# Kernel optimization log

Hardware: AMD Instinct MI355X
Metric: run time of the kernel (lower is better)

## Reference

```python
import jax, jax.numpy as jnp
import numpy as np
from jax import lax

B, S, D, H = 256, 512, 64, 128


def _cell(x, h, c, Wih, Whh, bih, bhh):
    # PyTorch LSTM gate layout: i, f, g, o
    g = x @ Wih.T + h @ Whh.T + (bih + bhh)
    i, f, gg, o = jnp.split(g, 4, axis=-1)
    c = jax.nn.sigmoid(f) * c + jax.nn.sigmoid(i) * jnp.tanh(gg)
    h = jax.nn.sigmoid(o) * jnp.tanh(c)
    return h, c


def _lstm_layer(xs, Wih, Whh, bih, bhh):
    # xs: [B, S, in] -> ys: [B, S, H], final (h, c): [B, H]
    b = xs.shape[0]
    h0 = jnp.zeros((b, H), xs.dtype)
    c0 = jnp.zeros((b, H), xs.dtype)

    def step(carry, xt):
        h, c = carry
        h, c = _cell(xt, h, c, Wih, Whh, bih, bhh)
        return (h, c), h

    (h, c), ys = lax.scan(step, (h0, c0), jnp.swapaxes(xs, 0, 1))
    return jnp.swapaxes(ys, 0, 1), h, c


def setup_inputs() -> dict:
    key = jax.random.key(0)
    ks = jax.random.split(key, 20)
    s = 1.0 / np.sqrt(H)
    p = {}
    p["x"] = jax.random.normal(ks[0], (B, S, D), jnp.float32)
    # encoder / decoder stacked LSTM params (layer 0 input=D, layer 1 input=H)
    idx = 1
    for pre in ["enc", "dec"]:
        for l, in_sz in [(0, D), (1, H)]:
            p[f"{pre}_Wih{l}"] = jax.random.uniform(ks[idx], (4 * H, in_sz), jnp.float32, -s, s); idx += 1
            p[f"{pre}_Whh{l}"] = jax.random.uniform(ks[idx], (4 * H, H), jnp.float32, -s, s); idx += 1
            p[f"{pre}_bih{l}"] = jax.random.uniform(ks[idx], (4 * H,), jnp.float32, -s, s); idx += 1
            p[f"{pre}_bhh{l}"] = jax.random.uniform(ks[idx], (4 * H,), jnp.float32, -s, s); idx += 1
    p["fc_W"] = jax.random.uniform(ks[17], (D, H), jnp.float32, -s, s)
    p["fc_b"] = jax.random.uniform(ks[18], (D,), jnp.float32, -s, s)
    return p


def reference(x, enc_Wih0, enc_Whh0, enc_bih0, enc_bhh0,
              enc_Wih1, enc_Whh1, enc_bih1, enc_bhh1,
              dec_Wih0, dec_Whh0, dec_bih0, dec_bhh0,
              dec_Wih1, dec_Whh1, dec_bih1, dec_bhh1,
              fc_W, fc_b):
    b, seq, d = x.shape
    # ---- Encoder: 2-layer LSTM (eval mode; inter-layer dropout disabled) ----
    y0, h0, c0 = _lstm_layer(x, enc_Wih0, enc_Whh0, enc_bih0, enc_bhh0)
    _, h1, c1 = _lstm_layer(y0, enc_Wih1, enc_Whh1, enc_bih1, enc_bhh1)

    def dec_step(carry, _):
        y, dh0, dc0, dh1, dc1 = carry
        dh0, dc0 = _cell(y, dh0, dc0, dec_Wih0, dec_Whh0, dec_bih0, dec_bhh0)
        dh1, dc1 = _cell(dh0, dh1, dc1, dec_Wih1, dec_Whh1, dec_bih1, dec_bhh1)
        pred = dh1 @ fc_W.T + fc_b
        return (pred, dh0, dc0, dh1, dc1), pred

    y_init = jnp.zeros((b, d), x.dtype)
    _, preds = lax.scan(dec_step, (y_init, h0, c0, h1, c1), None, length=seq)
    return jnp.swapaxes(preds, 0, 1)  # [B, S, D]
```

## Files before the change

### kernel.cpp

```cpp
#include <hip/hip_runtime.h>
#include <hip/hip_fp16.h>


typedef _Float16 h2 __attribute__((ext_vector_type(2)));
typedef _Float16 h8 __attribute__((ext_vector_type(8)));

#define Bsz 256
#define Ssz 512
#define Dsz 64
#define Hsz 128
#define G4 512
#define NT 512

__device__ __forceinline__ float fdot2f(h2 a, h2 b, float c) {
#if __has_builtin(__builtin_amdgcn_fdot2)
  return __builtin_amdgcn_fdot2(a, b, c, false);
#else
  return c + (float)a[0] * (float)b[0] + (float)a[1] * (float)b[1];
#endif
}

__device__ __forceinline__ float dot8(h8 v, h8 w, float acc) {
  h2 v0 = __builtin_shufflevector(v, v, 0, 1);
  h2 v1 = __builtin_shufflevector(v, v, 2, 3);
  h2 v2 = __builtin_shufflevector(v, v, 4, 5);
  h2 v3 = __builtin_shufflevector(v, v, 6, 7);
  h2 w0 = __builtin_shufflevector(w, w, 0, 1);
  h2 w1 = __builtin_shufflevector(w, w, 2, 3);
  h2 w2 = __builtin_shufflevector(w, w, 4, 5);
  h2 w3 = __builtin_shufflevector(w, w, 6, 7);
  acc = fdot2f(v0, w0, acc);
  acc = fdot2f(v1, w1, acc);
  acc = fdot2f(v2, w2, acc);
  acc = fdot2f(v3, w3, acc);
  return acc;
}

__device__ __forceinline__ float sigm(float v) { return 1.f / (1.f + __expf(-v)); }
__device__ __forceinline__ float tanh_f(float v) { return 2.f / (1.f + __expf(-2.f * v)) - 1.f; }

__global__ void __launch_bounds__(NT, 2)
enc_kernel(const float* __restrict__ x,
           const h8* __restrict__ wih0, const h8* __restrict__ whh0,
           const h8* __restrict__ wih1, const h8* __restrict__ whh1,
           const float* __restrict__ bsum0, const float* __restrict__ bsum1,
           float* __restrict__ st) {
  __shared__ h8 s_whh1[16 * G4];
  __shared__ float g[G4];
  __shared__ h8 hp0[16], hp1[16];
  __shared__ h8 xp[2][8];

  const int tid = threadIdx.x;
  const int row = blockIdx.x;

  h8 Wih0[8], Whh0[16], Wih1[16];
#pragma unroll
  for (int k = 0; k < 8; ++k) Wih0[k] = wih0[k * G4 + tid];
#pragma unroll
  for (int k = 0; k < 16; ++k) Whh0[k] = whh0[k * G4 + tid];
#pragma unroll
  for (int k = 0; k < 16; ++k) Wih1[k] = wih1[k * G4 + tid];
  for (int i = tid; i < 16 * G4; i += NT) s_whh1[i] = whh1[i];

  if (tid < 128) ((_Float16*)hp0)[tid] = (_Float16)0.f;
  else if (tid < 256) ((_Float16*)hp1)[tid - 128] = (_Float16)0.f;
  else if (tid < 320) {
    int j = tid - 256;
    ((_Float16*)xp[0])[j] = (_Float16)x[(size_t)row * Ssz * Dsz + j];
  }
  const float b0 = bsum0[tid];
  const float b1 = bsum1[tid];
  float c_reg = 0.f, h_last = 0.f;
  __syncthreads();

  for (int t = 0; t < Ssz; ++t) {
    {
      float a[4] = {b0, 0.f, 0.f, 0.f};
#pragma unroll
      for (int k = 0; k < 8; ++k) a[k & 3] = dot8(xp[t & 1][k], Wih0[k], a[k & 3]);
#pragma unroll
      for (int k = 0; k < 16; ++k) a[k & 3] = dot8(hp0[k], Whh0[k], a[k & 3]);
      g[4 * (tid & 127) + (tid >> 7)] = (a[0] + a[1]) + (a[2] + a[3]);
    }
    __syncthreads();
    if (tid < 128) {
      const float4 gv = *(const float4*)&g[4 * tid];
      float ig = sigm(gv.x), fg = sigm(gv.y), gg = tanh_f(gv.z), og = sigm(gv.w);
      c_reg = fg * c_reg + ig * gg;
      float h = og * tanh_f(c_reg);
      h_last = h;
      ((_Float16*)hp0)[tid] = (_Float16)h;
    } else if (tid >= 256 && tid < 320) {
      if (t + 1 < Ssz) {
        int j = tid - 256;
        ((_Float16*)xp[(t + 1) & 1])[j] =
            (_Float16)x[((size_t)row * Ssz + (t + 1)) * Dsz + j];
      }
    }
    __syncthreads();
    {
      float a[4] = {b1, 0.f, 0.f, 0.f};
#pragma unroll
      for (int k = 0; k < 16; ++k) a[k & 3] = dot8(hp0[k], Wih1[k], a[k & 3]);
#pragma unroll
      for (int k = 0; k < 16; ++k) a[k & 3] = dot8(hp1[k], s_whh1[k * G4 + tid], a[k & 3]);
      g[4 * (tid & 127) + (tid >> 7)] = (a[0] + a[1]) + (a[2] + a[3]);
    }
    __syncthreads();
    if (tid >= 128 && tid < 256) {
      int j = tid - 128;
      const float4 gv = *(const float4*)&g[4 * j];
      float ig = sigm(gv.x), fg = sigm(gv.y), gg = tanh_f(gv.z), og = sigm(gv.w);
      c_reg = fg * c_reg + ig * gg;
      float h = og * tanh_f(c_reg);
      h_last = h;
      ((_Float16*)hp1)[j] = (_Float16)h;
    }
    __syncthreads();
  }

  if (tid < 128) {
    st[0 * Bsz * Hsz + row * Hsz + tid] = h_last;
    st[1 * Bsz * Hsz + row * Hsz + tid] = c_reg;
  } else if (tid < 256) {
    int j = tid - 128;
    st[2 * Bsz * Hsz + row * Hsz + j] = h_last;
    st[3 * Bsz * Hsz + row * Hsz + j] = c_reg;
  }
}

__global__ void __launch_bounds__(NT, 2)
dec_kernel(const h8* __restrict__ wih0, const h8* __restrict__ whh0,
           const h8* __restrict__ wih1, const h8* __restrict__ whh1,
           const h8* __restrict__ fcp,
           const float* __restrict__ bsum0, const float* __restrict__ bsum1,
           const float* __restrict__ fcb, const float* __restrict__ st,
           float* __restrict__ out) {
  __shared__ h8 s_whh1[16 * G4];
  __shared__ h8 s_fc[16 * Dsz];
  __shared__ float g[G4];
  __shared__ h8 hp0[16], hp1[16], yp[8];

  const int tid = threadIdx.x;
  const int row = blockIdx.x;

  h8 Wih0[8], Whh0[16], Wih1[16];
#pragma unroll
  for (int k = 0; k < 8; ++k) Wih0[k] = wih0[k * G4 + tid];
#pragma unroll
  for (int k = 0; k < 16; ++k) Whh0[k] = whh0[k * G4 + tid];
#pragma unroll
  for (int k = 0; k < 16; ++k) Wih1[k] = wih1[k * G4 + tid];
  for (int i = tid; i < 16 * G4; i += NT) s_whh1[i] = whh1[i];
  for (int i = tid; i < 16 * Dsz; i += NT) s_fc[i] = fcp[i];

  float c_reg = 0.f;
  if (tid < 128) {
    float h0v = st[0 * Bsz * Hsz + row * Hsz + tid];
    c_reg = st[1 * Bsz * Hsz + row * Hsz + tid];
    ((_Float16*)hp0)[tid] = (_Float16)h0v;
  } else if (tid < 256) {
    int j = tid - 128;
    float h1v = st[2 * Bsz * Hsz + row * Hsz + j];
    c_reg = st[3 * Bsz * Hsz + row * Hsz + j];
    ((_Float16*)hp1)[j] = (_Float16)h1v;
  } else if (tid < 320) {
    ((_Float16*)yp)[tid - 256] = (_Float16)0.f;
  }
  const float b0 = bsum0[tid];
  const float b1 = bsum1[tid];
  const float fb = (tid < Dsz) ? fcb[tid] : 0.f;
  __syncthreads();

  for (int t = 0; t < Ssz; ++t) {
    {
      float a[4] = {b0, 0.f, 0.f, 0.f};
#pragma unroll
      for (int k = 0; k < 8; ++k) a[k & 3] = dot8(yp[k], Wih0[k], a[k & 3]);
#pragma unroll
      for (int k = 0; k < 16; ++k) a[k & 3] = dot8(hp0[k], Whh0[k], a[k & 3]);
      g[4 * (tid & 127) + (tid >> 7)] = (a[0] + a[1]) + (a[2] + a[3]);
    }
    __syncthreads();
    if (tid < 128) {
      const float4 gv = *(const float4*)&g[4 * tid];
      float ig = sigm(gv.x), fg = sigm(gv.y), gg = tanh_f(gv.z), og = sigm(gv.w);
      c_reg = fg * c_reg + ig * gg;
      float h = og * tanh_f(c_reg);
      ((_Float16*)hp0)[tid] = (_Float16)h;
    }
    __syncthreads();
    {
      float a[4] = {b1, 0.f, 0.f, 0.f};
#pragma unroll
      for (int k = 0; k < 16; ++k) a[k & 3] = dot8(hp0[k], Wih1[k], a[k & 3]);
#pragma unroll
      for (int k = 0; k < 16; ++k) a[k & 3] = dot8(hp1[k], s_whh1[k * G4 + tid], a[k & 3]);
      g[4 * (tid & 127) + (tid >> 7)] = (a[0] + a[1]) + (a[2] + a[3]);
    }
    __syncthreads();
    if (tid >= 128 && tid < 256) {
      int j = tid - 128;
      const float4 gv = *(const float4*)&g[4 * j];
      float ig = sigm(gv.x), fg = sigm(gv.y), gg = tanh_f(gv.z), og = sigm(gv.w);
      c_reg = fg * c_reg + ig * gg;
      float h = og * tanh_f(c_reg);
      ((_Float16*)hp1)[j] = (_Float16)h;
    }
    __syncthreads();
    if (tid < Dsz) {
      float a[2] = {fb, 0.f};
#pragma unroll
      for (int k = 0; k < 16; ++k) a[k & 1] = dot8(hp1[k], s_fc[k * Dsz + tid], a[k & 1]);
      float v = a[0] + a[1];
      out[((size_t)row * Ssz + t) * Dsz + tid] = v;
      ((_Float16*)yp)[tid] = (_Float16)v;
    }
    __syncthreads();
  }
}

__global__ void pack8_kernel(const float* __restrict__ W, h8* __restrict__ o, int K, int N) {
  int idx = blockIdx.x * 256 + threadIdx.x;
  int tot = (K >> 3) * N;
  if (idx >= tot) return;
  int k8 = idx / N, n = idx - k8 * N;
  const float* p = W + n * K + 8 * k8;
  h8 v;
#pragma unroll
  for (int j = 0; j < 8; ++j) v[j] = (_Float16)p[j];
  o[idx] = v;
}

__global__ void addb_kernel(const float* __restrict__ a, const float* __restrict__ b,
                            float* __restrict__ o, int n) {
  int i = blockIdx.x * 256 + threadIdx.x;
  if (i < n) o[i] = a[i] + b[i];
}

extern "C" void kernel_launch(void* const* d_in, const int* in_sizes, int n_in,
                              void* d_out, int out_size, void* d_ws, size_t ws_size,
                              hipStream_t stream) {
  (void)in_sizes; (void)n_in; (void)out_size; (void)ws_size;
  char* ws = (char*)d_ws;
  size_t off = 0;
  auto take = [&](size_t bytes) {
    char* p = ws + off;
    off += (bytes + 255) & ~(size_t)255;
    return p;
  };

  h8* e0_wih = (h8*)take(8 * 512 * 16);
  h8* e0_whh = (h8*)take(16 * 512 * 16);
  h8* e1_wih = (h8*)take(16 * 512 * 16);
  h8* e1_whh = (h8*)take(16 * 512 * 16);
  h8* d0_wih = (h8*)take(8 * 512 * 16);
  h8* d0_whh = (h8*)take(16 * 512 * 16);
  h8* d1_wih = (h8*)take(16 * 512 * 16);
  h8* d1_whh = (h8*)take(16 * 512 * 16);
  h8* fcp    = (h8*)take(16 * 64 * 16);
  float* bs_e0 = (float*)take(512 * 4);
  float* bs_e1 = (float*)take(512 * 4);
  float* bs_d0 = (float*)take(512 * 4);
  float* bs_d1 = (float*)take(512 * 4);
  float* st    = (float*)take(4 * Bsz * Hsz * 4);

  const float* x = (const float*)d_in[0];

  struct PW { const float* w; h8* o; int K, N; };
  PW pw[9] = {
    {(const float*)d_in[1],  e0_wih, 64, 512},
    {(const float*)d_in[2],  e0_whh, 128, 512},
    {(const float*)d_in[5],  e1_wih, 128, 512},
    {(const float*)d_in[6],  e1_whh, 128, 512},
    {(const float*)d_in[9],  d0_wih, 64, 512},
    {(const float*)d_in[10], d0_whh, 128, 512},
    {(const float*)d_in[13], d1_wih, 128, 512},
    {(const float*)d_in[14], d1_whh, 128, 512},
    {(const float*)d_in[17], fcp, 128, 64},
  };
  for (int i = 0; i < 9; ++i) {
    int tot = (pw[i].K >> 3) * pw[i].N;
    pack8_kernel<<<(tot + 255) / 256, 256, 0, stream>>>(pw[i].w, pw[i].o, pw[i].K, pw[i].N);
  }
  addb_kernel<<<2, 256, 0, stream>>>((const float*)d_in[3],  (const float*)d_in[4],  bs_e0, 512);
  addb_kernel<<<2, 256, 0, stream>>>((const float*)d_in[7],  (const float*)d_in[8],  bs_e1, 512);
  addb_kernel<<<2, 256, 0, stream>>>((const float*)d_in[11], (const float*)d_in[12], bs_d0, 512);
  addb_kernel<<<2, 256, 0, stream>>>((const float*)d_in[15], (const float*)d_in[16], bs_d1, 512);

  enc_kernel<<<Bsz, NT, 0, stream>>>(x, e0_wih, e0_whh, e1_wih, e1_whh, bs_e0, bs_e1, st);
  dec_kernel<<<Bsz, NT, 0, stream>>>(d0_wih, d0_whh, d1_wih, d1_whh, fcp, bs_d0, bs_d1,
                                     (const float*)d_in[18], st, (float*)d_out);
}
```

Baseline: 2.339 ms.

## Fold FC into decoder input weights and compute gates with DPP lane exchange

New measurement: 6.362 ms. 2.72x slower.

```diff
diff --git a/kernel.cpp b/kernel.cpp
--- a/kernel.cpp
+++ b/kernel.cpp
@@ -39,203 +39,251 @@
 __device__ __forceinline__ float sigm(float v) { return 1.f / (1.f + __expf(-v)); }
 __device__ __forceinline__ float tanh_f(float v) { return 2.f / (1.f + __expf(-2.f * v)) - 1.f; }
 
+template <int C, int M>
+__device__ __forceinline__ float qperm(float x) {
+#if __has_builtin(__builtin_amdgcn_mov_dpp)
+  int i = __builtin_amdgcn_mov_dpp(__builtin_bit_cast(int, x), C, 0xf, 0xf, true);
+  return __builtin_bit_cast(float, i);
+#else
+  return __shfl_xor(x, M, 64);
+#endif
+}
+
+__device__ __forceinline__ int permcol(int n) { return (n & 3) * 128 + (n >> 2); }
+
 __global__ void __launch_bounds__(NT, 2)
 enc_kernel(const float* __restrict__ x,
            const h8* __restrict__ wih0, const h8* __restrict__ whh0,
            const h8* __restrict__ wih1, const h8* __restrict__ whh1,
-           const float* __restrict__ bsum0, const float* __restrict__ bsum1,
+           const float* __restrict__ b0v, const float* __restrict__ b1v,
            float* __restrict__ st) {
-  __shared__ h8 s_whh1[16 * G4];
-  __shared__ float g[G4];
-  __shared__ h8 hp0[16], hp1[16];
-  __shared__ h8 xp[2][8];
+  __shared__ h8 s_wih0[8 * G4];
+  __shared__ h8 H0[2][16], H1[2][16], xp[2][8];
 
   const int tid = threadIdx.x;
   const int row = blockIdx.x;
-
-  h8 Wih0[8], Whh0[16], Wih1[16];
-#pragma unroll
-  for (int k = 0; k < 8; ++k) Wih0[k] = wih0[k * G4 + tid];
+  const int r = tid & 3;
+  const int j = tid >> 2;
+
+  h8 Whh0[16], Wih1[16], Whh1[16];
 #pragma unroll
   for (int k = 0; k < 16; ++k) Whh0[k] = whh0[k * G4 + tid];
 #pragma unroll
   for (int k = 0; k < 16; ++k) Wih1[k] = wih1[k * G4 + tid];
-  for (int i = tid; i < 16 * G4; i += NT) s_whh1[i] = whh1[i];
-
-  if (tid < 128) ((_Float16*)hp0)[tid] = (_Float16)0.f;
-  else if (tid < 256) ((_Float16*)hp1)[tid - 128] = (_Float16)0.f;
-  else if (tid < 320) {
-    int j = tid - 256;
-    ((_Float16*)xp[0])[j] = (_Float16)x[(size_t)row * Ssz * Dsz + j];
-  }
-  const float b0 = bsum0[tid];
-  const float b1 = bsum1[tid];
-  float c_reg = 0.f, h_last = 0.f;
+#pragma unroll
+  for (int k = 0; k < 16; ++k) Whh1[k] = whh1[k * G4 + tid];
+  for (int i = tid; i < 8 * G4; i += NT) s_wih0[i] = wih0[i];
+
+  if (tid < 128) ((_Float16*)H0[0])[tid] = (_Float16)0.f;
+  else if (tid < 256) ((_Float16*)H1[0])[tid - 128] = (_Float16)0.f;
+  else if (tid < 320)
+    ((_Float16*)xp[0])[tid - 256] = (_Float16)x[(size_t)row * Ssz * Dsz + (tid - 256)];
+
+  const float b0 = b0v[tid], b1 = b1v[tid];
+  const float Sc = (r == 2) ? 2.f : 1.f;
+  const float Kc = (r == 2) ? 2.f : 1.f;
+  const float Dc = (r == 2) ? -1.f : 0.f;
+  float c0 = 0.f, c1 = 0.f, h0_last = 0.f, h1_last = 0.f;
   __syncthreads();
 
   for (int t = 0; t < Ssz; ++t) {
-    {
-      float a[4] = {b0, 0.f, 0.f, 0.f};
-#pragma unroll
-      for (int k = 0; k < 8; ++k) a[k & 3] = dot8(xp[t & 1][k], Wih0[k], a[k & 3]);
-#pragma unroll
-      for (int k = 0; k < 16; ++k) a[k & 3] = dot8(hp0[k], Whh0[k], a[k & 3]);
-      g[4 * (tid & 127) + (tid >> 7)] = (a[0] + a[1]) + (a[2] + a[3]);
+    const h8* H0r = H0[t & 1];
+    h8* H0w = H0[(t + 1) & 1];
+    float xv = 0.f;
+    const bool pf = (tid < Dsz) && (t + 1 < Ssz);
+    if (pf) xv = x[((size_t)row * Ssz + (t + 1)) * Dsz + tid];
+    float a = b0;
+#pragma unroll
+    for (int k = 0; k < 8; ++k) a = dot8(xp[t & 1][k], s_wih0[k * G4 + tid], a);
+#pragma unroll
+    for (int k = 0; k < 16; ++k) a = dot8(H0r[k], Whh0[k], a);
+    if (pf) ((_Float16*)xp[(t + 1) & 1])[tid] = (_Float16)xv;
+    float n = Sc * sigm(Kc * a) + Dc;
+    float vf = qperm<0xB1, 1>(n), vg = qperm<0x4E, 2>(n), vo = qperm<0x1B, 3>(n);
+    if (r == 0) {
+      c0 = vf * c0 + n * vg;
+      float h = vo * tanh_f(c0);
+      h0_last = h;
+      ((_Float16*)H0w)[j] = (_Float16)h;
     }
     __syncthreads();
-    if (tid < 128) {
-      const float4 gv = *(const float4*)&g[4 * tid];
-      float ig = sigm(gv.x), fg = sigm(gv.y), gg = tanh_f(gv.z), og = sigm(gv.w);
-      c_reg = fg * c_reg + ig * gg;
-      float h = og * tanh_f(c_reg);
-      h_last = h;
-      ((_Float16*)hp0)[tid] = (_Float16)h;
-    } else if (tid >= 256 && tid < 320) {
-      if (t + 1 < Ssz) {
-        int j = tid - 256;
-        ((_Float16*)xp[(t + 1) & 1])[j] =
-            (_Float16)x[((size_t)row * Ssz + (t + 1)) * Dsz + j];
-      }
-    }
-    __syncthreads();
-    {
-      float a[4] = {b1, 0.f, 0.f, 0.f};
-#pragma unroll
-      for (int k = 0; k < 16; ++k) a[k & 3] = dot8(hp0[k], Wih1[k], a[k & 3]);
-#pragma unroll
-      for (int k = 0; k < 16; ++k) a[k & 3] = dot8(hp1[k], s_whh1[k * G4 + tid], a[k & 3]);
-      g[4 * (tid & 127) + (tid >> 7)] = (a[0] + a[1]) + (a[2] + a[3]);
-    }
-    __syncthreads();
-    if (tid >= 128 && tid < 256) {
-      int j = tid - 128;
-      const float4 gv = *(const float4*)&g[4 * j];
-      float ig = sigm(gv.x), fg = sigm(gv.y), gg = tanh_f(gv.z), og = sigm(gv.w);
-      c_reg = fg * c_reg + ig * gg;
-      float h = og * tanh_f(c_reg);
-      h_last = h;
-      ((_Float16*)hp1)[j] = (_Float16)h;
-    }
-    __syncthreads();
-  }
-
-  if (tid < 128) {
-    st[0 * Bsz * Hsz + row * Hsz + tid] = h_last;
-    st[1 * Bsz * Hsz + row * Hsz + tid] = c_reg;
-  } else if (tid < 256) {
-    int j = tid - 128;
-    st[2 * Bsz * Hsz + row * Hsz + j] = h_last;
-    st[3 * Bsz * Hsz + row * Hsz + j] = c_reg;
+    const h8* H1r = H1[t & 1];
+    h8* H1w = H1[(t + 1) & 1];
+    float a1 = b1;
+#pragma unroll
+    for (int k = 0; k < 16; ++k) a1 = dot8(H0w[k], Wih1[k], a1);
+#pragma unroll
+    for (int k = 0; k < 16; ++k) a1 = dot8(H1r[k], Whh1[k], a1);
+    n = Sc * sigm(Kc * a1) + Dc;
+    vf = qperm<0xB1, 1>(n); vg = qperm<0x4E, 2>(n); vo = qperm<0x1B, 3>(n);
+    if (r == 0) {
+      c1 = vf * c1 + n * vg;
+      float h = vo * tanh_f(c1);
+      h1_last = h;
+      ((_Float16*)H1w)[j] = (_Float16)h;
+    }
+  }
+  if (r == 0) {
+    st[0 * Bsz * Hsz + row * Hsz + j] = h0_last;
+    st[1 * Bsz * Hsz + row * Hsz + j] = c0;
+    st[2 * Bsz * Hsz + row * Hsz + j] = h1_last;
+    st[3 * Bsz * Hsz + row * Hsz + j] = c1;
   }
 }
 
 __global__ void __launch_bounds__(NT, 2)
-dec_kernel(const h8* __restrict__ wih0, const h8* __restrict__ whh0,
+dec_kernel(const h8* __restrict__ wprime, const h8* __restrict__ whh0,
            const h8* __restrict__ wih1, const h8* __restrict__ whh1,
-           const h8* __restrict__ fcp,
-           const float* __restrict__ bsum0, const float* __restrict__ bsum1,
-           const float* __restrict__ fcb, const float* __restrict__ st,
-           float* __restrict__ out) {
+           const h8* __restrict__ fcpk,
+           const float* __restrict__ b00v, const float* __restrict__ b0tv,
+           const float* __restrict__ b1v, const float* __restrict__ fcb,
+           const float* __restrict__ st, float* __restrict__ out) {
   __shared__ h8 s_whh1[16 * G4];
-  __shared__ h8 s_fc[16 * Dsz];
-  __shared__ float g[G4];
-  __shared__ h8 hp0[16], hp1[16], yp[8];
+  __shared__ h8 H0[2][16], H1[2][16];
 
   const int tid = threadIdx.x;
   const int row = blockIdx.x;
-
-  h8 Wih0[8], Whh0[16], Wih1[16];
-#pragma unroll
-  for (int k = 0; k < 8; ++k) Wih0[k] = wih0[k * G4 + tid];
+  const int r = tid & 3;
+  const int j = tid >> 2;
+  const int j8 = tid >> 3;
+  const int kp = (tid & 7) * 2;
+
+  h8 Wp[16], Whh0[16], Wih1[16];
+#pragma unroll
+  for (int k = 0; k < 16; ++k) Wp[k] = wprime[k * G4 + tid];
 #pragma unroll
   for (int k = 0; k < 16; ++k) Whh0[k] = whh0[k * G4 + tid];
 #pragma unroll
   for (int k = 0; k < 16; ++k) Wih1[k] = wih1[k * G4 + tid];
+  const h8 Fc0 = fcpk[tid * 2];
+  const h8 Fc1 = fcpk[tid * 2 + 1];
   for (int i = tid; i < 16 * G4; i += NT) s_whh1[i] = whh1[i];
-  for (int i = tid; i < 16 * Dsz; i += NT) s_fc[i] = fcp[i];
-
-  float c_reg = 0.f;
-  if (tid < 128) {
-    float h0v = st[0 * Bsz * Hsz + row * Hsz + tid];
-    c_reg = st[1 * Bsz * Hsz + row * Hsz + tid];
-    ((_Float16*)hp0)[tid] = (_Float16)h0v;
-  } else if (tid < 256) {
-    int j = tid - 128;
-    float h1v = st[2 * Bsz * Hsz + row * Hsz + j];
-    c_reg = st[3 * Bsz * Hsz + row * Hsz + j];
-    ((_Float16*)hp1)[j] = (_Float16)h1v;
-  } else if (tid < 320) {
-    ((_Float16*)yp)[tid - 256] = (_Float16)0.f;
-  }
-  const float b0 = bsum0[tid];
-  const float b1 = bsum1[tid];
-  const float fb = (tid < Dsz) ? fcb[tid] : 0.f;
+
+  float c0 = 0.f, c1 = 0.f;
+  if (tid < 128)
+    ((_Float16*)H0[0])[tid] = (_Float16)st[0 * Bsz * Hsz + row * Hsz + tid];
+  else if (tid < 256)
+    ((_Float16*)H1[0])[tid - 128] = (_Float16)st[2 * Bsz * Hsz + row * Hsz + (tid - 128)];
+  if (r == 0) {
+    c0 = st[1 * Bsz * Hsz + row * Hsz + j];
+    c1 = st[3 * Bsz * Hsz + row * Hsz + j];
+  }
+  const float b00 = b00v[tid], b0t = b0tv[tid], b1 = b1v[tid];
+  const float fcbj = fcb[j8];
+  const float Sc = (r == 2) ? 2.f : 1.f;
+  const float Kc = (r == 2) ? 2.f : 1.f;
+  const float Dc = (r == 2) ? -1.f : 0.f;
   __syncthreads();
 
   for (int t = 0; t < Ssz; ++t) {
-    {
-      float a[4] = {b0, 0.f, 0.f, 0.f};
-#pragma unroll
-      for (int k = 0; k < 8; ++k) a[k & 3] = dot8(yp[k], Wih0[k], a[k & 3]);
-#pragma unroll
-      for (int k = 0; k < 16; ++k) a[k & 3] = dot8(hp0[k], Whh0[k], a[k & 3]);
-      g[4 * (tid & 127) + (tid >> 7)] = (a[0] + a[1]) + (a[2] + a[3]);
+    const h8* H0r = H0[t & 1];
+    h8* H0w = H0[(t + 1) & 1];
+    const h8* H1r = H1[t & 1];
+    float a;
+    if (t > 0) {
+      a = b0t;
+#pragma unroll
+      for (int k = 0; k < 16; ++k) a = dot8(H1r[k], Wp[k], a);
+      float op = dot8(H1r[kp], Fc0, 0.f);
+      op = dot8(H1r[kp + 1], Fc1, op);
+      op += __shfl_xor(op, 1);
+      op += __shfl_xor(op, 2);
+      op += __shfl_xor(op, 4);
+      if ((tid & 7) == 0)
+        out[((size_t)row * Ssz + (t - 1)) * Dsz + j8] = op + fcbj;
+    } else {
+      a = b00;
+    }
+#pragma unroll
+    for (int k = 0; k < 16; ++k) a = dot8(H0r[k], Whh0[k], a);
+    float n = Sc * sigm(Kc * a) + Dc;
+    float vf = qperm<0xB1, 1>(n), vg = qperm<0x4E, 2>(n), vo = qperm<0x1B, 3>(n);
+    if (r == 0) {
+      c0 = vf * c0 + n * vg;
+      ((_Float16*)H0w)[j] = (_Float16)(vo * tanh_f(c0));
     }
     __syncthreads();
-    if (tid < 128) {
-      const float4 gv = *(const float4*)&g[4 * tid];
-      float ig = sigm(gv.x), fg = sigm(gv.y), gg = tanh_f(gv.z), og = sigm(gv.w);
-      c_reg = fg * c_reg + ig * gg;
-      float h = og * tanh_f(c_reg);
-      ((_Float16*)hp0)[tid] = (_Float16)h;
+    h8* H1w = H1[(t + 1) & 1];
+    float a1 = b1;
+#pragma unroll
+    for (int k = 0; k < 16; ++k) a1 = dot8(H0w[k], Wih1[k], a1);
+#pragma unroll
+    for (int k = 0; k < 16; ++k) a1 = dot8(H1r[k], s_whh1[k * G4 + tid], a1);
+    n = Sc * sigm(Kc * a1) + Dc;
+    vf = qperm<0xB1, 1>(n); vg = qperm<0x4E, 2>(n); vo = qperm<0x1B, 3>(n);
+    if (r == 0) {
+      c1 = vf * c1 + n * vg;
+      ((_Float16*)H1w)[j] = (_Float16)(vo * tanh_f(c1));
     }
     __syncthreads();
-    {
-      float a[4] = {b1, 0.f, 0.f, 0.f};
-#pragma unroll
-      for (int k = 0; k < 16; ++k) a[k & 3] = dot8(hp0[k], Wih1[k], a[k & 3]);
-#pragma unroll
-      for (int k = 0; k < 16; ++k) a[k & 3] = dot8(hp1[k], s_whh1[k * G4 + tid], a[k & 3]);
-      g[4 * (tid & 127) + (tid >> 7)] = (a[0] + a[1]) + (a[2] + a[3]);
-    }
-    __syncthreads();
-    if (tid >= 128 && tid < 256) {
-      int j = tid - 128;
-      const float4 gv = *(const float4*)&g[4 * j];
-      float ig = sigm(gv.x), fg = sigm(gv.y), gg = tanh_f(gv.z), og = sigm(gv.w);
-      c_reg = fg * c_reg + ig * gg;
-      float h = og * tanh_f(c_reg);
-      ((_Float16*)hp1)[j] = (_Float16)h;
-    }
-    __syncthreads();
-    if (tid < Dsz) {
-      float a[2] = {fb, 0.f};
-#pragma unroll
-      for (int k = 0; k < 16; ++k) a[k & 1] = dot8(hp1[k], s_fc[k * Dsz + tid], a[k & 1]);
-      float v = a[0] + a[1];
-      out[((size_t)row * Ssz + t) * Dsz + tid] = v;
-      ((_Float16*)yp)[tid] = (_Float16)v;
-    }
-    __syncthreads();
-  }
-}
-
-__global__ void pack8_kernel(const float* __restrict__ W, h8* __restrict__ o, int K, int N) {
+  }
+  const h8* H1f = H1[Ssz & 1];
+  float op = dot8(H1f[kp], Fc0, 0.f);
+  op = dot8(H1f[kp + 1], Fc1, op);
+  op += __shfl_xor(op, 1);
+  op += __shfl_xor(op, 2);
+  op += __shfl_xor(op, 4);
+  if ((tid & 7) == 0)
+    out[((size_t)row * Ssz + (Ssz - 1)) * Dsz + j8] = op + fcbj;
+}
+
+
+__global__ void pack8p_kernel(const float* __restrict__ W, h8* __restrict__ o, int K) {
   int idx = blockIdx.x * 256 + threadIdx.x;
-  int tot = (K >> 3) * N;
+  int tot = (K >> 3) * G4;
   if (idx >= tot) return;
-  int k8 = idx / N, n = idx - k8 * N;
-  const float* p = W + n * K + 8 * k8;
+  int k8 = idx >> 9, np = idx & 511;
+  const float* p = W + permcol(np) * K + 8 * k8;
   h8 v;
 #pragma unroll
-  for (int j = 0; j < 8; ++j) v[j] = (_Float16)p[j];
+  for (int e = 0; e < 8; ++e) v[e] = (_Float16)p[e];
   o[idx] = v;
 }
 
-__global__ void addb_kernel(const float* __restrict__ a, const float* __restrict__ b,
-                            float* __restrict__ o, int n) {
-  int i = blockIdx.x * 256 + threadIdx.x;
-  if (i < n) o[i] = a[i] + b[i];
+__global__ void wprime_kernel(const float* __restrict__ wih0d, const float* __restrict__ fcw,
+                              h8* __restrict__ o) {
+  int idx = blockIdx.x * 256 + threadIdx.x;
+  if (idx >= 16 * G4) return;
+  int k8 = idx >> 9, np = idx & 511;
+  int col = permcol(np);
+  h8 v;
+#pragma unroll
+  for (int e = 0; e < 8; ++e) {
+    int h = 8 * k8 + e;
+    float s = 0.f;
+    for (int d = 0; d < 64; ++d) s += wih0d[col * 64 + d] * fcw[d * 128 + h];
+    v[e] = (_Float16)s;
+  }
+  o[idx] = v;
+}
+
+__global__ void fcpack_kernel(const float* __restrict__ fcw, h8* __restrict__ o) {
+  int idx = blockIdx.x * 256 + threadIdx.x;
+  if (idx >= 2 * NT) return;
+  int tt = idx >> 1, c = idx & 1;
+  int jj = tt >> 3, k = (tt & 7) * 2 + c;
+  h8 v;
+#pragma unroll
+  for (int e = 0; e < 8; ++e) v[e] = (_Float16)fcw[jj * 128 + k * 8 + e];
+  o[idx] = v;
+}
+
+__global__ void biasp_kernel(const float* __restrict__ a, const float* __restrict__ b,
+                             float* __restrict__ o) {
+  int n = blockIdx.x * 256 + threadIdx.x;
+  if (n >= G4) return;
+  int c = permcol(n);
+  o[n] = a[c] + b[c];
+}
+
+__global__ void bprime_kernel(const float* __restrict__ b00, const float* __restrict__ wih0d,
+                              const float* __restrict__ fcb, float* __restrict__ o) {
+  int n = blockIdx.x * 256 + threadIdx.x;
+  if (n >= G4) return;
+  int c = permcol(n);
+  float s = 0.f;
+  for (int d = 0; d < 64; ++d) s += fcb[d] * wih0d[c * 64 + d];
+  o[n] = b00[n] + s;
 }
 
 extern "C" void kernel_launch(void* const* d_in, const int* in_sizes, int n_in,
@@ -254,41 +302,38 @@
   h8* e0_whh = (h8*)take(16 * 512 * 16);
   h8* e1_wih = (h8*)take(16 * 512 * 16);
   h8* e1_whh = (h8*)take(16 * 512 * 16);
-  h8* d0_wih = (h8*)take(8 * 512 * 16);
+  h8* d_wp   = (h8*)take(16 * 512 * 16);
   h8* d0_whh = (h8*)take(16 * 512 * 16);
   h8* d1_wih = (h8*)take(16 * 512 * 16);
   h8* d1_whh = (h8*)take(16 * 512 * 16);
-  h8* fcp    = (h8*)take(16 * 64 * 16);
-  float* bs_e0 = (float*)take(512 * 4);
-  float* bs_e1 = (float*)take(512 * 4);
-  float* bs_d0 = (float*)take(512 * 4);
-  float* bs_d1 = (float*)take(512 * 4);
+  h8* fcpk   = (h8*)take(2 * 512 * 16);
+  float* b_e0  = (float*)take(512 * 4);
+  float* b_e1  = (float*)take(512 * 4);
+  float* b_d00 = (float*)take(512 * 4);
+  float* b_d0t = (float*)take(512 * 4);
+  float* b_d1  = (float*)take(512 * 4);
   float* st    = (float*)take(4 * Bsz * Hsz * 4);
 
   const float* x = (const float*)d_in[0];
 
-  struct PW { const float* w; h8* o; int K, N; };
-  PW pw[9] = {
-    {(const float*)d_in[1],  e0_wih, 64, 512},
-    {(const float*)d_in[2],  e0_whh, 128, 512},
-    {(const float*)d_in[5],  e1_wih, 128, 512},
-    {(const float*)d_in[6],  e1_whh, 128, 512},
-    {(const float*)d_in[9],  d0_wih, 64, 512},
-    {(const float*)d_in[10], d0_whh, 128, 512},
-    {(const float*)d_in[13], d1_wih, 128, 512},
-    {(const float*)d_in[14], d1_whh, 128, 512},
-    {(const float*)d_in[17], fcp, 128, 64},
-  };
-  for (int i = 0; i < 9; ++i) {
-    int tot = (pw[i].K >> 3) * pw[i].N;
-    pack8_kernel<<<(tot + 255) / 256, 256, 0, stream>>>(pw[i].w, pw[i].o, pw[i].K, pw[i].N);
-  }
-  addb_kernel<<<2, 256, 0, stream>>>((const float*)d_in[3],  (const float*)d_in[4],  bs_e0, 512);
-  addb_kernel<<<2, 256, 0, stream>>>((const float*)d_in[7],  (const float*)d_in[8],  bs_e1, 512);
-  addb_kernel<<<2, 256, 0, stream>>>((const float*)d_in[11], (const float*)d_in[12], bs_d0, 512);
-  addb_kernel<<<2, 256, 0, stream>>>((const float*)d_in[15], (const float*)d_in[16], bs_d1, 512);
-
-  enc_kernel<<<Bsz, NT, 0, stream>>>(x, e0_wih, e0_whh, e1_wih, e1_whh, bs_e0, bs_e1, st);
-  dec_kernel<<<Bsz, NT, 0, stream>>>(d0_wih, d0_whh, d1_wih, d1_whh, fcp, bs_d0, bs_d1,
-                                     (const float*)d_in[18], st, (float*)d_out);
-}
+  pack8p_kernel<<<16, 256, 0, stream>>>((const float*)d_in[1], e0_wih, 64);
+  pack8p_kernel<<<32, 256, 0, stream>>>((const float*)d_in[2], e0_whh, 128);
+  pack8p_kernel<<<32, 256, 0, stream>>>((const float*)d_in[5], e1_wih, 128);
+  pack8p_kernel<<<32, 256, 0, stream>>>((const float*)d_in[6], e1_whh, 128);
+  wprime_kernel<<<32, 256, 0, stream>>>((const float*)d_in[9], (const float*)d_in[17], d_wp);
+  pack8p_kernel<<<32, 256, 0, stream>>>((const float*)d_in[10], d0_whh, 128);
+  pack8p_kernel<<<32, 256, 0, stream>>>((const float*)d_in[13], d1_wih, 128);
+  pack8p_kernel<<<32, 256, 0, stream>>>((const float*)d_in[14], d1_whh, 128);
+  fcpack_kernel<<<4, 256, 0, stream>>>((const float*)d_in[17], fcpk);
+
+  biasp_kernel<<<2, 256, 0, stream>>>((const float*)d_in[3], (const float*)d_in[4], b_e0);
+  biasp_kernel<<<2, 256, 0, stream>>>((const float*)d_in[7], (const float*)d_in[8], b_e1);
+  biasp_kernel<<<2, 256, 0, stream>>>((const float*)d_in[11], (const float*)d_in[12], b_d00);
+  biasp_kernel<<<2, 256, 0, stream>>>((const float*)d_in[15], (const float*)d_in[16], b_d1);
+  bprime_kernel<<<2, 256, 0, stream>>>(b_d00, (const float*)d_in[9], (const float*)d_in[18], b_d0t);
+
+  enc_kernel<<<Bsz, NT, 0, stream>>>(x, e0_wih, e0_whh, e1_wih, e1_whh, b_e0, b_e1, st);
+  dec_kernel<<<Bsz, NT, 0, stream>>>(d_wp, d0_whh, d1_wih, d1_whh, fcpk,
+                                     b_d00, b_d0t, b_d1, (const float*)d_in[18], st,
+                                     (float*)d_out);
+}
```
